# Kernel optimization log

Measured on AMD Instinct MI355X. Metric: run time of the kernel, lower is better.

Reference implementation:

```python
import jax, jax.numpy as jnp
import numpy as np

N_NODES = 100000
N_EDGES = 1600000
D_IN = 256
D_OUT = 128


def setup_inputs() -> dict:
    key = jax.random.key(0)
    ks = jax.random.split(key, 7)
    h = jax.random.normal(ks[0], (N_NODES, D_IN), dtype=jnp.float32)
    src = jax.random.randint(ks[1], (N_EDGES,), 0, N_NODES, dtype=jnp.int32)
    dst = jax.random.randint(ks[2], (N_EDGES,), 0, N_NODES, dtype=jnp.int32)
    W = jax.random.normal(ks[3], (D_IN, D_OUT), dtype=jnp.float32) * (1.0 / np.sqrt(D_IN))
    b = jax.random.normal(ks[4], (D_OUT,), dtype=jnp.float32) * 0.01
    w_att = jax.random.normal(ks[5], (2 * D_OUT, 1), dtype=jnp.float32) * (1.0 / np.sqrt(2 * D_OUT))
    b_att = jax.random.normal(ks[6], (1,), dtype=jnp.float32) * 0.01
    return {"h": h, "src": src, "dst": dst, "W": W, "b": b, "w_att": w_att, "b_att": b_att}


def reference(h, src, dst, W, b, w_att, b_att):
    # node projection: graph.ndata['h'] = self.linear(h)
    hp = h @ W + b  # [N, D_OUT]
    n = hp.shape[0]
    d = hp.shape[1]
    # edge attention: leaky_relu(att_linear(cat[h_src, h_dst]))
    # cat([hs, hd]) @ w_att == hs @ w_att[:d] + hd @ w_att[d:]  (avoids [E, 2d] concat)
    wa_s = w_att[:d, 0]  # [D_OUT]
    wa_d = w_att[d:, 0]  # [D_OUT]
    e = hp[src] @ wa_s + hp[dst] @ wa_d + b_att[0]  # [E]
    e = jax.nn.leaky_relu(e)  # default negative_slope 0.01 matches F.leaky_relu
    # segment softmax over each destination node's incoming edges
    emax = jax.ops.segment_max(e, dst, num_segments=n)  # [N]
    ex = jnp.exp(e - emax[dst])  # [E]
    denom = jax.ops.segment_sum(ex, dst, num_segments=n)  # [N]
    # weighted scatter-sum of src features: sum_e alpha_e * h_src_e
    num = jax.ops.segment_sum(ex[:, None] * hp[src], dst, num_segments=n)  # [N, D_OUT]
    out = num / jnp.where(denom > 0, denom, 1.0)[:, None]  # zero-in-degree nodes -> 0
    return out
```

## Files before the change

### kernel.cpp

```cpp
#include <hip/hip_runtime.h>
#include <hip/hip_bf16.h>

#define D_IN 256
#define D_OUT 128
#define BNODES 64
#define BCAP 1536
#define EPB 8192
#define MAXNB 1600

typedef __attribute__((ext_vector_type(8))) short bf16x8;
typedef __attribute__((ext_vector_type(4))) float f32x4;

__device__ __forceinline__ unsigned short f2bf(float f) {
    unsigned u = __float_as_uint(f);
    unsigned r = ((u >> 16) & 1u) + 0x7FFFu;
    return (unsigned short)((u + r) >> 16);
}
__device__ __forceinline__ unsigned pk2(float a, float b) {
    return (unsigned)f2bf(a) | ((unsigned)f2bf(b) << 16);
}
__device__ __forceinline__ bf16x8 pack8(float4 a, float4 b) {
    union { uint4 u; bf16x8 v; } r;
    r.u.x = pk2(a.x, a.y); r.u.y = pk2(a.z, a.w);
    r.u.z = pk2(b.x, b.y); r.u.w = pk2(b.z, b.w);
    return r.v;
}
__device__ __forceinline__ void gload_lds16(const void* g, void* l) {
    __builtin_amdgcn_global_load_lds(
        (const __attribute__((address_space(1))) void*)g,
        (__attribute__((address_space(3))) void*)l, 16, 0, 0);
}

__global__ __launch_bounds__(256) void init_bcursor_kernel(int* __restrict__ bcursor, int nb)
{
    int i = blockIdx.x * 256 + threadIdx.x;
    if (i < nb) bcursor[i] = i * BCAP;
}

__global__ __launch_bounds__(256) void prep_kernel(
    const float* __restrict__ W, unsigned short* __restrict__ WbT)
{
    int idx = blockIdx.x * 256 + threadIdx.x;
    int k = idx >> 7;
    int c = idx & 127;
    WbT[(size_t)c * 256 + k] = f2bf(W[idx]);
}

__global__ __launch_bounds__(256, 2) void gemm_mfma_kernel(
    const float* __restrict__ h, const unsigned short* __restrict__ WbT,
    const float* __restrict__ b, const float* __restrict__ w_att,
    unsigned short* __restrict__ hpb,
    float* __restrict__ alpha_s, float* __restrict__ alpha_d, int n)
{
    __shared__ char bT[65536];
    const int t = threadIdx.x;
    const int wv = t >> 6, lane = t & 63;
    const int fr = lane & 15, fq = lane >> 4;
    const int r0 = blockIdx.x * 256 + wv * 64;
    const int swz = (fr & 7) << 4;

    {
        #pragma unroll
        for (int j = 0; j < 16; ++j) {
            int col = wv * 32 + j * 2 + (lane >> 5);
            int seg = lane & 31;
            const char* src = (const char*)WbT + col * 512 + ((seg * 16) ^ ((col & 7) << 4));
            char* dst = bT + (wv * 32 + j * 2) * 512;
            gload_lds16(src, dst);
        }
    }
    __syncthreads();

    const float* arow[4];
    #pragma unroll
    for (int m = 0; m < 4; ++m) {
        int rg = r0 + m * 16 + fr;
        if (rg >= n) rg = n - 1;
        arow[m] = h + (size_t)rg * D_IN + fq * 8;
    }

    f32x4 acc[4][8];
    #pragma unroll
    for (int m = 0; m < 4; ++m)
        #pragma unroll
        for (int nn = 0; nn < 8; ++nn) acc[m][nn] = (f32x4){0.f, 0.f, 0.f, 0.f};

    float4 bufA[2][4][2];
    #pragma unroll
    for (int m = 0; m < 4; ++m) {
        const float4* ap = (const float4*)arow[m];
        bufA[0][m][0] = ap[0]; bufA[0][m][1] = ap[1];
    }

    #pragma unroll
    for (int ks = 0; ks < 8; ++ks) {
        const int cur = ks & 1, nxt = cur ^ 1;
        if (ks < 7) {
            #pragma unroll
            for (int m = 0; m < 4; ++m) {
                const float4* ap = (const float4*)(arow[m] + (ks + 1) * 32);
                bufA[nxt][m][0] = ap[0]; bufA[nxt][m][1] = ap[1];
            }
        }
        bf16x8 af[4];
        #pragma unroll
        for (int m = 0; m < 4; ++m)
            af[m] = pack8(bufA[cur][m][0], bufA[cur][m][1]);

        #pragma unroll
        for (int nn = 0; nn < 8; ++nn) {
            bf16x8 bfr = *(const bf16x8*)(bT + nn * 8192 + fr * 512
                            + ((ks * 64 + fq * 16) ^ swz));
            #pragma unroll
            for (int m = 0; m < 4; ++m)
                acc[m][nn] = __builtin_amdgcn_mfma_f32_16x16x32_bf16(
                    af[m], bfr, acc[m][nn], 0, 0, 0);
        }
    }

    float bcol[8], was[8], wad[8];
    #pragma unroll
    for (int nn = 0; nn < 8; ++nn) {
        int j = nn * 16 + fr;
        bcol[nn] = b[j]; was[nn] = w_att[j]; wad[nn] = w_att[D_OUT + j];
    }
    #pragma unroll
    for (int m = 0; m < 4; ++m) {
        #pragma unroll
        for (int reg = 0; reg < 4; ++reg) {
            const int grow = r0 + m * 16 + fq * 4 + reg;
            const bool ok = grow < n;
            float ps = 0.f, pd = 0.f;
            #pragma unroll
            for (int nn = 0; nn < 8; ++nn) {
                float vv = acc[m][nn][reg] + bcol[nn];
                ps += vv * was[nn];
                pd += vv * wad[nn];
                if (ok) hpb[(size_t)grow * D_OUT + nn * 16 + fr] = f2bf(vv);
            }
            #pragma unroll
            for (int o = 1; o < 16; o <<= 1) {
                ps += __shfl_xor(ps, o);
                pd += __shfl_xor(pd, o);
            }
            if (fr == 0 && ok) { alpha_s[grow] = ps; alpha_d[grow] = pd; }
        }
    }
}

__global__ __launch_bounds__(1024) void bucket_scatter_kernel(
    const int* __restrict__ src, const int* __restrict__ dst,
    const float* __restrict__ alpha_s, const float* __restrict__ alpha_d,
    const float* __restrict__ b_att, int* __restrict__ bcursor,
    int2* __restrict__ ebuf, int ne, int nb)
{
    __shared__ int lhist[MAXNB];
    __shared__ int gbase[MAXNB];
    __shared__ int lcur[MAXNB];
    const int t = threadIdx.x;
    for (int i = t; i < nb; i += 1024) { lhist[i] = 0; lcur[i] = 0; }
    __syncthreads();
    const int base = blockIdx.x * EPB;
    #pragma unroll
    for (int j = 0; j < EPB / 1024; ++j) {
        int idx = base + j * 1024 + t;
        if (idx < ne) atomicAdd(&lhist[dst[idx] >> 6], 1);
    }
    __syncthreads();
    for (int i = t; i < nb; i += 1024) {
        int c = lhist[i];
        gbase[i] = c ? atomicAdd(&bcursor[i], c) : 0;
    }
    __syncthreads();
    const float ba = b_att[0];
    #pragma unroll
    for (int j = 0; j < EPB / 1024; ++j) {
        int idx = base + j * 1024 + t;
        if (idx < ne) {
            int s = src[idx], d = dst[idx];
            float ev = alpha_s[s] + alpha_d[d] + ba;
            ev = (ev >= 0.f) ? ev : 0.01f * ev;
            int bkt = d >> 6;
            int pos = gbase[bkt] + atomicAdd(&lcur[bkt], 1);
            if (pos < (bkt + 1) * BCAP)
                ebuf[pos] = make_int2(s | ((d & 63) << 17), __float_as_int(ev));
        }
    }
}

#define ACCUM8(uvar, wvar)                                     \
    acc[0] += (wvar) * __uint_as_float((uvar).x << 16);        \
    acc[1] += (wvar) * __uint_as_float((uvar).x & 0xFFFF0000u);\
    acc[2] += (wvar) * __uint_as_float((uvar).y << 16);        \
    acc[3] += (wvar) * __uint_as_float((uvar).y & 0xFFFF0000u);\
    acc[4] += (wvar) * __uint_as_float((uvar).z << 16);        \
    acc[5] += (wvar) * __uint_as_float((uvar).z & 0xFFFF0000u);\
    acc[6] += (wvar) * __uint_as_float((uvar).w << 16);        \
    acc[7] += (wvar) * __uint_as_float((uvar).w & 0xFFFF0000u);

__global__ __launch_bounds__(512) void aggregate_kernel(
    const unsigned short* __restrict__ hpb, const int2* __restrict__ ebuf,
    const int* __restrict__ bcursor, float* __restrict__ out, int n)
{
    __shared__ int2 srec[BCAP];
    __shared__ int lhist[BNODES], lstart[BNODES], lcur[BNODES];
    const int t = threadIdx.x;
    const int bk = blockIdx.x;
    const int node0 = bk << 6;
    const int base = bk * BCAP;
    int cnt = bcursor[bk] - base;
    cnt = min(cnt, BCAP);

    if (t < BNODES) lhist[t] = 0;
    __syncthreads();
    for (int i = t; i < cnt; i += 512)
        atomicAdd(&lhist[(ebuf[base + i].x >> 17) & 63], 1);
    __syncthreads();
    if (t < BNODES) {
        int c0 = lhist[t];
        int incl = c0;
        #pragma unroll
        for (int o = 1; o < 64; o <<= 1) {
            int v = __shfl_up(incl, o);
            if (t >= o) incl += v;
        }
        lstart[t] = incl - c0;
        lcur[t]   = incl - c0;
    }
    __syncthreads();
    for (int i = t; i < cnt; i += 512) {
        int2 r = ebuf[base + i];
        int pos = atomicAdd(&lcur[(r.x >> 17) & 63], 1);
        srec[pos] = r;
    }
    __syncthreads();

    const int wv = t >> 6, lane = t & 63;
    const int q = lane >> 4, dlane = lane & 15;
    const uint4* hp4 = (const uint4*)hpb;

    #pragma unroll
    for (int p = 0; p < 2; ++p) {
        const int nd = p * 32 + wv * 4 + q;
        const int gnode = node0 + nd;
        const int off = lstart[nd], c = lhist[nd];

        float m = -INFINITY;
        for (int i = dlane; i < c; i += 16)
            m = fmaxf(m, __int_as_float(srec[off + i].y));
        #pragma unroll
        for (int o = 8; o; o >>= 1) m = fmaxf(m, __shfl_xor(m, o));

        float acc[8] = {0.f,0.f,0.f,0.f,0.f,0.f,0.f,0.f};
        float denom = 0.f;

        for (int t0 = 0; t0 < c; t0 += 4) {
            const int cm1 = c - 1;
            int2 r0 = srec[off + min(t0 + 0, cm1)];
            int2 r1 = srec[off + min(t0 + 1, cm1)];
            int2 r2 = srec[off + min(t0 + 2, cm1)];
            int2 r3 = srec[off + min(t0 + 3, cm1)];
            float w0 = __expf(__int_as_float(r0.y) - m);
            float w1 = (t0 + 1 < c) ? __expf(__int_as_float(r1.y) - m) : 0.f;
            float w2 = (t0 + 2 < c) ? __expf(__int_as_float(r2.y) - m) : 0.f;
            float w3 = (t0 + 3 < c) ? __expf(__int_as_float(r3.y) - m) : 0.f;
            uint4 u0 = hp4[(size_t)(r0.x & 0x1FFFF) * 16 + dlane];
            uint4 u1 = hp4[(size_t)(r1.x & 0x1FFFF) * 16 + dlane];
            uint4 u2 = hp4[(size_t)(r2.x & 0x1FFFF) * 16 + dlane];
            uint4 u3 = hp4[(size_t)(r3.x & 0x1FFFF) * 16 + dlane];
            ACCUM8(u0, w0) denom += w0;
            ACCUM8(u1, w1) denom += w1;
            ACCUM8(u2, w2) denom += w2;
            ACCUM8(u3, w3) denom += w3;
        }

        if (gnode < n) {
            float inv = (c > 0) ? 1.f / denom : 0.f;
            float4 o0 = { acc[0]*inv, acc[1]*inv, acc[2]*inv, acc[3]*inv };
            float4 o1 = { acc[4]*inv, acc[5]*inv, acc[6]*inv, acc[7]*inv };
            float4* op = (float4*)(out + (size_t)gnode * D_OUT) + 2 * dlane;
            op[0] = o0;
            op[1] = o1;
        }
    }
}

extern "C" void kernel_launch(void* const* d_in, const int* in_sizes, int n_in,
                              void* d_out, int out_size, void* d_ws, size_t ws_size,
                              hipStream_t stream)
{
    const float* h     = (const float*)d_in[0];
    const int*   src   = (const int*)  d_in[1];
    const int*   dst   = (const int*)  d_in[2];
    const float* W     = (const float*)d_in[3];
    const float* b     = (const float*)d_in[4];
    const float* w_att = (const float*)d_in[5];
    const float* b_att = (const float*)d_in[6];
    float* out = (float*)d_out;

    const int n  = in_sizes[0] / D_IN;
    const int ne = in_sizes[1];
    const int nb = (n + BNODES - 1) / BNODES;

    unsigned short* hpb = (unsigned short*)d_ws;
    float* alpha_s = (float*)d_ws + (size_t)n * 64;
    float* alpha_d = alpha_s + n;
    int2*  ebuf    = (int2*)(alpha_d + n);
    int*   bcursor = (int*)(ebuf + (size_t)nb * BCAP);
    unsigned short* WbT = (unsigned short*)(bcursor + nb);

    init_bcursor_kernel<<<(nb + 255) / 256, 256, 0, stream>>>(bcursor, nb);
    prep_kernel<<<128, 256, 0, stream>>>(W, WbT);
    gemm_mfma_kernel<<<(n + 255) / 256, 256, 0, stream>>>(
        h, WbT, b, w_att, hpb, alpha_s, alpha_d, n);
    bucket_scatter_kernel<<<(ne + EPB - 1) / EPB, 1024, 0, stream>>>(
        src, dst, alpha_s, alpha_d, b_att, bcursor, ebuf, ne, nb);
    aggregate_kernel<<<nb, 512, 0, stream>>>(hpb, ebuf, bcursor, out, n);
}
```

Baseline: 137.3 us.

## Halve GEMM tile and LDS footprint, stage W in two K halves; shrink aggregate blocks

The projection GEMM now computes 128 rows per block (32 per wave) instead of 256, and stages only half of the transposed bf16 weight matrix (32 KB) in LDS at a time, reloading the second K half midway with extra barriers. The smaller LDS and register footprint allows three blocks per CU and doubles the grid, aiming for better latency hiding and a smaller tail. The aggregate kernel drops from 512 to 256 threads per block, with each wave handling four node passes instead of two. In exchange the GEMM reuses each B fragment across fewer rows, reads W from L2 twice per block, and adds a mid-loop synchronization.

```diff
diff --git a/kernel.cpp b/kernel.cpp
--- a/kernel.cpp
+++ b/kernel.cpp
@@ -46,75 +46,83 @@
     WbT[(size_t)c * 256 + k] = f2bf(W[idx]);
 }
 
-__global__ __launch_bounds__(256, 2) void gemm_mfma_kernel(
+__global__ __launch_bounds__(256, 3) void gemm_mfma_kernel(
     const float* __restrict__ h, const unsigned short* __restrict__ WbT,
     const float* __restrict__ b, const float* __restrict__ w_att,
     unsigned short* __restrict__ hpb,
     float* __restrict__ alpha_s, float* __restrict__ alpha_d, int n)
 {
-    __shared__ char bT[65536];
+    __shared__ char bT[32768];
     const int t = threadIdx.x;
     const int wv = t >> 6, lane = t & 63;
     const int fr = lane & 15, fq = lane >> 4;
-    const int r0 = blockIdx.x * 256 + wv * 64;
+    const int r0 = blockIdx.x * 128 + wv * 32;
     const int swz = (fr & 7) << 4;
 
-    {
-        #pragma unroll
-        for (int j = 0; j < 16; ++j) {
-            int col = wv * 32 + j * 2 + (lane >> 5);
-            int seg = lane & 31;
-            const char* src = (const char*)WbT + col * 512 + ((seg * 16) ^ ((col & 7) << 4));
-            char* dst = bT + (wv * 32 + j * 2) * 512;
-            gload_lds16(src, dst);
-        }
-    }
-    __syncthreads();
-
-    const float* arow[4];
-    #pragma unroll
-    for (int m = 0; m < 4; ++m) {
+    const int scol = wv * 32 + (lane >> 4) - ((lane >> 4) & 3) * 0;
+    auto stage = [&](int hh) {
+        #pragma unroll
+        for (int j = 0; j < 8; ++j) {
+            int col0 = wv * 32 + j * 4;
+            int col = col0 + (lane >> 4);
+            int seg = lane & 15;
+            const char* src = (const char*)WbT + col * 512 + hh * 256
+                            + ((seg * 16) ^ ((col & 7) << 4));
+            gload_lds16(src, bT + col0 * 256);
+        }
+    };
+    (void)scol;
+
+    stage(0);
+
+    const float* arow[2];
+    #pragma unroll
+    for (int m = 0; m < 2; ++m) {
         int rg = r0 + m * 16 + fr;
         if (rg >= n) rg = n - 1;
         arow[m] = h + (size_t)rg * D_IN + fq * 8;
     }
 
-    f32x4 acc[4][8];
-    #pragma unroll
-    for (int m = 0; m < 4; ++m)
+    f32x4 acc[2][8];
+    #pragma unroll
+    for (int m = 0; m < 2; ++m)
         #pragma unroll
         for (int nn = 0; nn < 8; ++nn) acc[m][nn] = (f32x4){0.f, 0.f, 0.f, 0.f};
 
-    float4 bufA[2][4][2];
-    #pragma unroll
-    for (int m = 0; m < 4; ++m) {
+    float4 bufA[2][2][2];
+    #pragma unroll
+    for (int m = 0; m < 2; ++m) {
         const float4* ap = (const float4*)arow[m];
         bufA[0][m][0] = ap[0]; bufA[0][m][1] = ap[1];
     }
-
-    #pragma unroll
-    for (int ks = 0; ks < 8; ++ks) {
-        const int cur = ks & 1, nxt = cur ^ 1;
-        if (ks < 7) {
+    __syncthreads();
+
+    #pragma unroll
+    for (int kk = 0; kk < 8; ++kk) {
+        if (kk == 4) {
+            __syncthreads();
+            stage(1);
+            __syncthreads();
+        }
+        const int cur = kk & 1, nxt = cur ^ 1;
+        if (kk < 7) {
             #pragma unroll
-            for (int m = 0; m < 4; ++m) {
-                const float4* ap = (const float4*)(arow[m] + (ks + 1) * 32);
+            for (int m = 0; m < 2; ++m) {
+                const float4* ap = (const float4*)(arow[m] + (kk + 1) * 32);
                 bufA[nxt][m][0] = ap[0]; bufA[nxt][m][1] = ap[1];
             }
         }
-        bf16x8 af[4];
-        #pragma unroll
-        for (int m = 0; m < 4; ++m)
+        bf16x8 af[2];
+        #pragma unroll
+        for (int m = 0; m < 2; ++m)
             af[m] = pack8(bufA[cur][m][0], bufA[cur][m][1]);
 
+        const int x = (kk & 3) * 64 + fq * 16;
         #pragma unroll
         for (int nn = 0; nn < 8; ++nn) {
-            bf16x8 bfr = *(const bf16x8*)(bT + nn * 8192 + fr * 512
-                            + ((ks * 64 + fq * 16) ^ swz));
-            #pragma unroll
-            for (int m = 0; m < 4; ++m)
-                acc[m][nn] = __builtin_amdgcn_mfma_f32_16x16x32_bf16(
-                    af[m], bfr, acc[m][nn], 0, 0, 0);
+            bf16x8 bfr = *(const bf16x8*)(bT + (nn * 16 + fr) * 256 + (x ^ swz));
+            acc[0][nn] = __builtin_amdgcn_mfma_f32_16x16x32_bf16(af[0], bfr, acc[0][nn], 0, 0, 0);
+            acc[1][nn] = __builtin_amdgcn_mfma_f32_16x16x32_bf16(af[1], bfr, acc[1][nn], 0, 0, 0);
         }
     }
 
@@ -125,7 +133,7 @@
         bcol[nn] = b[j]; was[nn] = w_att[j]; wad[nn] = w_att[D_OUT + j];
     }
     #pragma unroll
-    for (int m = 0; m < 4; ++m) {
+    for (int m = 0; m < 2; ++m) {
         #pragma unroll
         for (int reg = 0; reg < 4; ++reg) {
             const int grow = r0 + m * 16 + fq * 4 + reg;
@@ -198,7 +206,7 @@
     acc[6] += (wvar) * __uint_as_float((uvar).w << 16);        \
     acc[7] += (wvar) * __uint_as_float((uvar).w & 0xFFFF0000u);
 
-__global__ __launch_bounds__(512) void aggregate_kernel(
+__global__ __launch_bounds__(256) void aggregate_kernel(
     const unsigned short* __restrict__ hpb, const int2* __restrict__ ebuf,
     const int* __restrict__ bcursor, float* __restrict__ out, int n)
 {
@@ -213,7 +221,7 @@
 
     if (t < BNODES) lhist[t] = 0;
     __syncthreads();
-    for (int i = t; i < cnt; i += 512)
+    for (int i = t; i < cnt; i += 256)
         atomicAdd(&lhist[(ebuf[base + i].x >> 17) & 63], 1);
     __syncthreads();
     if (t < BNODES) {
@@ -228,7 +236,7 @@
         lcur[t]   = incl - c0;
     }
     __syncthreads();
-    for (int i = t; i < cnt; i += 512) {
+    for (int i = t; i < cnt; i += 256) {
         int2 r = ebuf[base + i];
         int pos = atomicAdd(&lcur[(r.x >> 17) & 63], 1);
         srec[pos] = r;
@@ -240,8 +248,8 @@
     const uint4* hp4 = (const uint4*)hpb;
 
     #pragma unroll
-    for (int p = 0; p < 2; ++p) {
-        const int nd = p * 32 + wv * 4 + q;
+    for (int p = 0; p < 4; ++p) {
+        const int nd = p * 16 + wv * 4 + q;
         const int gnode = node0 + nd;
         const int off = lstart[nd], c = lhist[nd];
 
@@ -311,9 +319,9 @@
 
     init_bcursor_kernel<<<(nb + 255) / 256, 256, 0, stream>>>(bcursor, nb);
     prep_kernel<<<128, 256, 0, stream>>>(W, WbT);
-    gemm_mfma_kernel<<<(n + 255) / 256, 256, 0, stream>>>(
+    gemm_mfma_kernel<<<(n + 127) / 128, 256, 0, stream>>>(
         h, WbT, b, w_att, hpb, alpha_s, alpha_d, n);
     bucket_scatter_kernel<<<(ne + EPB - 1) / EPB, 1024, 0, stream>>>(
         src, dst, alpha_s, alpha_d, b_att, bcursor, ebuf, ne, nb);
-    aggregate_kernel<<<nb, 512, 0, stream>>>(hpb, ebuf, bcursor, out, n);
-}
+    aggregate_kernel<<<nb, 256, 0, stream>>>(hpb, ebuf, bcursor, out, n);
+}
```

Measured after the change: 139.5 us. About the same (+1.6%).
